# Kernel optimization log

Hardware: AMD Instinct MI355X
Metric: run time of the kernel (lower is better)

Reference implementation:

```python
import jax, jax.numpy as jnp
import numpy as np
import itertools

DIM = 384
KEY_DIM = 32
NUM_HEADS = 8
ATTN_RATIO = 4
RESOLUTION = 7
D = ATTN_RATIO * KEY_DIM          # 128
DH = D * NUM_HEADS                # 1024
H_QKV = DH + 2 * KEY_DIM * NUM_HEADS  # 1536
B = 2048
N = RESOLUTION ** 2               # 49


def _build_bias_idxs():
    points = list(itertools.product(range(RESOLUTION), range(RESOLUTION)))
    attention_offsets = {}
    idxs = []
    for p1 in points:
        for p2 in points:
            offset = (abs(p1[0] - p2[0]), abs(p1[1] - p2[1]))
            if offset not in attention_offsets:
                attention_offsets[offset] = len(attention_offsets)
            idxs.append(attention_offsets[offset])
    return np.array(idxs, dtype=np.int32).reshape(N, N), len(attention_offsets)


def setup_inputs() -> dict:
    key = jax.random.key(0)
    ks = jax.random.split(key, 6)
    bias_idxs_np, n_offsets = _build_bias_idxs()  # n_offsets == 49 for resolution 7
    x = jax.random.normal(ks[0], (B, N, DIM), dtype=jnp.float32)
    qkv_w = jax.random.normal(ks[1], (H_QKV, DIM), dtype=jnp.float32) * (DIM ** -0.5)
    qkv_b = jnp.zeros((H_QKV,), dtype=jnp.float32)
    proj_w = jax.random.normal(ks[2], (DIM, DH), dtype=jnp.float32) * (DH ** -0.5)
    proj_b = jnp.zeros((DIM,), dtype=jnp.float32)
    attn_bias = jax.random.normal(ks[3], (NUM_HEADS, n_offsets), dtype=jnp.float32) * 0.02
    bias_idxs = jnp.asarray(bias_idxs_np)
    return {"x": x, "qkv_w": qkv_w, "qkv_b": qkv_b, "proj_w": proj_w,
            "proj_b": proj_b, "attn_bias": attn_bias, "bias_idxs": bias_idxs}


def reference(x, qkv_w, qkv_b, proj_w, proj_b, attn_bias, bias_idxs):
    Bb, Nn, _ = x.shape
    scale = KEY_DIM ** -0.5
    qkv = x @ qkv_w.T + qkv_b                       # [B, N, 1536]
    qkv = qkv.reshape(Bb, Nn, NUM_HEADS, KEY_DIM + KEY_DIM + D)
    q = qkv[..., :KEY_DIM]                          # [B, N, H, kd]
    k = qkv[..., KEY_DIM:2 * KEY_DIM]               # [B, N, H, kd]
    v = qkv[..., 2 * KEY_DIM:]                      # [B, N, H, d]
    bias = attn_bias[:, bias_idxs]                  # [H, N, N] gathered rel-pos bias
    attn = jnp.einsum('bnhk,bmhk->bhnm', q, k) * scale + bias
    attn = jax.nn.softmax(attn, axis=-1)
    out = jnp.einsum('bhnm,bmhd->bnhd', attn, v).reshape(Bb, Nn, DH)
    return out @ proj_w.T + proj_b                  # [B, N, dim]
```

## Files before the change

kernel.cpp:

```cpp
#include <hip/hip_runtime.h>
#include <cstddef>
#include <cstdint>

#define TOK    49
#define KD     32
#define NH     8
#define DHEAD  128
#define HQKV   1536
#define DHTOT  1024
#define DIMM   384

typedef unsigned short u16;
typedef float  f32x4  __attribute__((ext_vector_type(4)));
typedef __bf16 bf16x8 __attribute__((ext_vector_type(8)));

typedef const __attribute__((address_space(1))) void gas_void;
typedef __attribute__((address_space(3))) void las_void;

static __device__ __forceinline__ u16 f2bf(float f) {
    unsigned int u = __builtin_bit_cast(unsigned int, f);
    return (u16)((u + 0x7fffu + ((u >> 16) & 1u)) >> 16);
}

static __device__ __forceinline__ int swz(int row, int c) {
    return (row << 6) + ((((c >> 3) ^ (row & 7)) << 3) | (c & 7));
}

static __device__ __forceinline__ int swzV(int row, int c) {
    return (row << 6) + ((((c >> 3) ^ (row & 7) ^ ((row >> 3) & 7)) << 3) | (c & 7));
}

static __device__ __forceinline__ int xcd_chunk(int bid, int nwg) {
    const int xcd = bid & 7, slot = bid >> 3;
    const int q = nwg >> 3, r = nwg & 7;
    return (xcd < r ? xcd * (q + 1) : r * (q + 1) + (xcd - r) * q) + slot;
}

#define BAR() __builtin_amdgcn_s_barrier()
#define WAIT_VM8() asm volatile("s_waitcnt vmcnt(8)" ::: "memory")
#define WAIT_VM0() asm volatile("s_waitcnt vmcnt(0)" ::: "memory")

__global__ __launch_bounds__(256)
void cast_swz(const float* __restrict__ in, u16* __restrict__ out, int K8, long nchunk)
{
    long i = (long)blockIdx.x * 256 + threadIdx.x;
    const long stride = (long)gridDim.x * 256;
    for (; i < nchunk; i += stride) {
        const long row = i / K8;
        const int  c8  = (int)(i - row * K8);
        const int  slot = c8 & 7, tpan = c8 >> 3;
        float4 v0 = reinterpret_cast<const float4*>(in)[i * 2];
        float4 v1 = reinterpret_cast<const float4*>(in)[i * 2 + 1];
        uint4 o;
        o.x = f2bf(v0.x) | ((unsigned)f2bf(v0.y) << 16);
        o.y = f2bf(v0.z) | ((unsigned)f2bf(v0.w) << 16);
        o.z = f2bf(v1.x) | ((unsigned)f2bf(v1.y) << 16);
        o.w = f2bf(v1.z) | ((unsigned)f2bf(v1.w) << 16);
        *reinterpret_cast<uint4*>(out + row * (long)K8 * 8 + tpan * 64 +
                                  ((slot ^ ((int)row & 7)) << 3)) = o;
    }
}

__global__ __launch_bounds__(256)
void bias_expand(const float* __restrict__ attn_bias, const int* __restrict__ idxs,
                 float* __restrict__ bias_full, int n_off)
{
    int i = blockIdx.x * 256 + threadIdx.x;
    if (i < NH * TOK * TOK) {
        int h = i / (TOK * TOK), s = i - h * (TOK * TOK);
        bias_full[i] = attn_bias[h * n_off + idxs[s]];
    }
}

static __device__ __forceinline__ int frag_off(int row, int ks8fg) {
    return (row << 6) + (((ks8fg ^ (row & 7)) << 3));
}

__global__ __launch_bounds__(256)
void gemm_qkv(const u16* __restrict__ A,
              const u16* __restrict__ W,
              const float* __restrict__ bias,
              u16* __restrict__ qkvb, int M)
{
    const int K = DIMM;
    const int NB = HQKV / 128;
    const int nwg = (M / 128) * NB;
    const int wgid = xcd_chunk(blockIdx.x, nwg);
    const int bm = (wgid / NB) * 128;
    const int bn = (wgid % NB) * 128;

    __shared__ u16 Alds[2][128 * 64];
    __shared__ u16 Blds[2][128 * 64];

    const int t    = threadIdx.x;
    const int lane = t & 63;
    const int wv   = t >> 6;
    const int wr   = wv >> 1;
    const int wc   = wv & 1;

    const int lrow = lane >> 3;
    const int lcol = (lane & 7) * 8;
    const int frow = lane & 15;
    const int fg   = lane >> 4;

    f32x4 acc[4][4];
    #pragma unroll
    for (int mi = 0; mi < 4; ++mi)
        #pragma unroll
        for (int ni = 0; ni < 4; ++ni) acc[mi][ni] = (f32x4)0.0f;

    auto STAGE = [&](int buf, int k0) {
        #pragma unroll
        for (int i = 0; i < 4; ++i) {
            const int c   = i * 4 + wv;
            const int row = c * 8 + lrow;
            __builtin_amdgcn_global_load_lds((gas_void*)(A + (size_t)(bm + row) * K + k0 + lcol),
                                             (las_void*)(&Alds[buf][c * 512]), 16, 0, 0);
            __builtin_amdgcn_global_load_lds((gas_void*)(W + (size_t)(bn + row) * K + k0 + lcol),
                                             (las_void*)(&Blds[buf][c * 512]), 16, 0, 0);
        }
    };

    STAGE(0, 0);
    STAGE(1, 64);

    const int NT = 6;
    for (int ts = 0; ts < NT; ++ts) {
        if (ts < NT - 1) { WAIT_VM8(); }
        else             { WAIT_VM0(); }
        BAR();
        const u16* Ab = Alds[ts & 1];
        const u16* Bb = Blds[ts & 1];
        #pragma unroll
        for (int ks = 0; ks < 2; ++ks) {
            const int sl = ks * 4 + fg;
            bf16x8 af[4], bf[4];
            #pragma unroll
            for (int mi = 0; mi < 4; ++mi)
                af[mi] = *reinterpret_cast<const bf16x8*>(&Ab[frag_off(wr * 64 + mi * 16 + frow, sl)]);
            #pragma unroll
            for (int ni = 0; ni < 4; ++ni)
                bf[ni] = *reinterpret_cast<const bf16x8*>(&Bb[frag_off(wc * 64 + ni * 16 + frow, sl)]);
            #pragma unroll
            for (int mi = 0; mi < 4; ++mi)
                #pragma unroll
                for (int ni = 0; ni < 4; ++ni)
                    acc[mi][ni] = __builtin_amdgcn_mfma_f32_16x16x32_bf16(af[mi], bf[ni], acc[mi][ni], 0, 0, 0);
        }
        BAR();
        if (ts < NT - 2) STAGE(ts & 1, (ts + 2) * 64);
    }

    const int rbase = (lane >> 4) * 4;
    #pragma unroll
    for (int ni = 0; ni < 4; ++ni) {
        const int col = bn + wc * 64 + ni * 16 + frow;
        const float bv = bias[col];
        #pragma unroll
        for (int mi = 0; mi < 4; ++mi) {
            #pragma unroll
            for (int j = 0; j < 4; ++j) {
                const int row = bm + wr * 64 + mi * 16 + rbase + j;
                qkvb[(size_t)row * HQKV + col] = f2bf(acc[mi][ni][j] + bv);
            }
        }
    }
}

__global__ __launch_bounds__(256)
void gemm_bf16_nt(const u16* __restrict__ A, const u16* __restrict__ W,
                  const float* __restrict__ bias, float* __restrict__ C,
                  int M, int N, int K)
{
    const int NB = N / 128;
    const int nwg = (M / 128) * NB;
    const int wgid = xcd_chunk(blockIdx.x, nwg);
    const int bm = (wgid / NB) * 128;
    const int bn = (wgid % NB) * 128;

    __shared__ u16 Alds[2][128 * 64];
    __shared__ u16 Blds[2][128 * 64];

    const int t    = threadIdx.x;
    const int lane = t & 63;
    const int wv   = t >> 6;
    const int wr   = wv >> 1;
    const int wc   = wv & 1;

    const int lrow = lane >> 3;
    const int lcol = (lane & 7) * 8;
    const int frow = lane & 15;
    const int fg   = lane >> 4;

    f32x4 acc[4][4];
    #pragma unroll
    for (int mi = 0; mi < 4; ++mi)
        #pragma unroll
        for (int ni = 0; ni < 4; ++ni) acc[mi][ni] = (f32x4)0.0f;

    auto STAGE = [&](int buf, int k0) {
        #pragma unroll
        for (int i = 0; i < 4; ++i) {
            const int c   = i * 4 + wv;
            const int row = c * 8 + lrow;
            __builtin_amdgcn_global_load_lds((gas_void*)(A + (size_t)(bm + row) * K + k0 + lcol),
                                             (las_void*)(&Alds[buf][c * 512]), 16, 0, 0);
            __builtin_amdgcn_global_load_lds((gas_void*)(W + (size_t)(bn + row) * K + k0 + lcol),
                                             (las_void*)(&Blds[buf][c * 512]), 16, 0, 0);
        }
    };

    const int NT = K / 64;
    STAGE(0, 0);
    STAGE(1, 64);

    for (int ts = 0; ts < NT; ++ts) {
        if (ts < NT - 1) { WAIT_VM8(); }
        else             { WAIT_VM0(); }
        BAR();
        const u16* Ab = Alds[ts & 1];
        const u16* Bb = Blds[ts & 1];
        #pragma unroll
        for (int ks = 0; ks < 2; ++ks) {
            const int sl = ks * 4 + fg;
            bf16x8 af[4], bf[4];
            #pragma unroll
            for (int mi = 0; mi < 4; ++mi)
                af[mi] = *reinterpret_cast<const bf16x8*>(&Ab[frag_off(wr * 64 + mi * 16 + frow, sl)]);
            #pragma unroll
            for (int ni = 0; ni < 4; ++ni)
                bf[ni] = *reinterpret_cast<const bf16x8*>(&Bb[frag_off(wc * 64 + ni * 16 + frow, sl)]);
            #pragma unroll
            for (int mi = 0; mi < 4; ++mi)
                #pragma unroll
                for (int ni = 0; ni < 4; ++ni)
                    acc[mi][ni] = __builtin_amdgcn_mfma_f32_16x16x32_bf16(af[mi], bf[ni], acc[mi][ni], 0, 0, 0);
        }
        BAR();
        if (ts < NT - 2) STAGE(ts & 1, (ts + 2) * 64);
    }

    const int rbase = (lane >> 4) * 4;
    #pragma unroll
    for (int ni = 0; ni < 4; ++ni) {
        const int col = bn + wc * 64 + ni * 16 + frow;
        const float bv = bias[col];
        #pragma unroll
        for (int mi = 0; mi < 4; ++mi) {
            #pragma unroll
            for (int j = 0; j < 4; ++j) {
                const int row = bm + wr * 64 + mi * 16 + rbase + j;
                C[(size_t)row * N + col] = acc[mi][ni][j] + bv;
            }
        }
    }
}

__global__ __launch_bounds__(256)
void attn_mfma(const u16* __restrict__ qkvb,
               const float* __restrict__ bias_full,
               u16* __restrict__ ab)
{
    __shared__ __align__(16) u16  QKs[64 * 64];
    __shared__ __align__(16) u16  Vts[128 * 64];
    __shared__ __align__(16) float S[64 * 80];
    __shared__ __align__(16) u16  Ps[64 * 64];

    const int t    = threadIdx.x;
    const int lane = t & 63;
    const int w    = t >> 6;
    const int fr   = lane & 15;
    const int fg   = lane >> 4;
    const int b    = blockIdx.x;
    const int h    = blockIdx.y;

    if (t < 128 * 2) {
        const int row = t >> 1, sl = 6 + (t & 1);
        *reinterpret_cast<uint4*>(&Vts[(row << 6) +
            (((sl ^ (row & 7) ^ ((row >> 3) & 7)) & 7) << 3)]) = make_uint4(0, 0, 0, 0);
    }
    __syncthreads();

    const u16* qrow = qkvb + (size_t)b * TOK * HQKV + h * 192;
    for (int flat = t; flat < TOK * 24; flat += 256) {
        const int n = flat / 24, c24 = flat - n * 24;
        uint4 u = *reinterpret_cast<const uint4*>(qrow + (size_t)n * HQKV + c24 * 8);
        if (c24 < 8) {
            *reinterpret_cast<uint4*>(&QKs[(n << 6) + ((c24 ^ (n & 7)) << 3)]) = u;
        } else {
            const int d0 = (c24 - 8) * 8;
            u16 vals[8];
            *reinterpret_cast<uint4*>(vals) = u;
            #pragma unroll
            for (int e = 0; e < 8; ++e)
                Vts[swzV(d0 + e, n)] = vals[e];
        }
    }
    __syncthreads();

    bf16x8 qf = *reinterpret_cast<const bf16x8*>(&QKs[swz(16 * w + fr, fg * 8)]);
    f32x4 sacc[4];
    #pragma unroll
    for (int nj = 0; nj < 4; ++nj) {
        bf16x8 kf = *reinterpret_cast<const bf16x8*>(&QKs[swz(16 * nj + fr, 32 + fg * 8)]);
        sacc[nj] = __builtin_amdgcn_mfma_f32_16x16x32_bf16(qf, kf, (f32x4)0.0f, 0, 0, 0);
    }

    const float scale = 0.17677669529663687f;
    const float* bh_bias = bias_full + h * (TOK * TOK);
    #pragma unroll
    for (int nj = 0; nj < 4; ++nj) {
        #pragma unroll
        for (int j = 0; j < 4; ++j) {
            const int row = 16 * w + fg * 4 + j;
            const int col = 16 * nj + fr;
            const int rn = row < TOK ? row : TOK - 1;
            const int cm = col < TOK ? col : TOK - 1;
            S[row * 80 + col] = sacc[nj][j] * scale + bh_bias[rn * TOK + cm];
        }
    }
    __syncthreads();

    {
        const int n = t >> 2, j = t & 3;
        const float* Sr = &S[n * 80];
        float v[16];
        #pragma unroll
        for (int e = 0; e < 8; ++e) v[e]     = Sr[8 * j + e];
        #pragma unroll
        for (int e = 0; e < 8; ++e) v[8 + e] = Sr[32 + 8 * j + e];

        float mx = -1e30f;
        #pragma unroll
        for (int e = 0; e < 8; ++e) mx = fmaxf(mx, v[e]);
        #pragma unroll
        for (int e = 0; e < 8; ++e)
            if (32 + 8 * j + e < TOK) mx = fmaxf(mx, v[8 + e]);
        mx = fmaxf(mx, __shfl_xor(mx, 1, 4));
        mx = fmaxf(mx, __shfl_xor(mx, 2, 4));

        float sum = 0.f;
        #pragma unroll
        for (int e = 0; e < 8; ++e) { v[e] = __expf(v[e] - mx); sum += v[e]; }
        #pragma unroll
        for (int e = 0; e < 8; ++e) {
            const float ev = (32 + 8 * j + e < TOK) ? __expf(v[8 + e] - mx) : 0.f;
            v[8 + e] = ev; sum += ev;
        }
        sum += __shfl_xor(sum, 1, 4);
        sum += __shfl_xor(sum, 2, 4);
        const float inv = 1.f / sum;

        uint4 o;
        o.x = f2bf(v[0] * inv)  | ((unsigned)f2bf(v[1] * inv)  << 16);
        o.y = f2bf(v[2] * inv)  | ((unsigned)f2bf(v[3] * inv)  << 16);
        o.z = f2bf(v[4] * inv)  | ((unsigned)f2bf(v[5] * inv)  << 16);
        o.w = f2bf(v[6] * inv)  | ((unsigned)f2bf(v[7] * inv)  << 16);
        *reinterpret_cast<uint4*>(&Ps[swz(n, 8 * j)]) = o;
        o.x = f2bf(v[8] * inv)  | ((unsigned)f2bf(v[9] * inv)  << 16);
        o.y = f2bf(v[10] * inv) | ((unsigned)f2bf(v[11] * inv) << 16);
        o.z = f2bf(v[12] * inv) | ((unsigned)f2bf(v[13] * inv) << 16);
        o.w = f2bf(v[14] * inv) | ((unsigned)f2bf(v[15] * inv) << 16);
        *reinterpret_cast<uint4*>(&Ps[swz(n, 32 + 8 * j)]) = o;
    }
    __syncthreads();

    f32x4 oacc[8];
    #pragma unroll
    for (int nj = 0; nj < 8; ++nj) oacc[nj] = (f32x4)0.0f;
    #pragma unroll
    for (int ks = 0; ks < 2; ++ks) {
        bf16x8 pf = *reinterpret_cast<const bf16x8*>(&Ps[swz(16 * w + fr, ks * 32 + fg * 8)]);
        #pragma unroll
        for (int nj = 0; nj < 8; ++nj) {
            bf16x8 vf = *reinterpret_cast<const bf16x8*>(&Vts[swzV(16 * nj + fr, ks * 32 + fg * 8)]);
            oacc[nj] = __builtin_amdgcn_mfma_f32_16x16x32_bf16(pf, vf, oacc[nj], 0, 0, 0);
        }
    }

    #pragma unroll
    for (int nj = 0; nj < 8; ++nj) {
        const int d = 16 * nj + fr;
        const int c = h * DHEAD + d;
        const int tp = c >> 6, sl = (c >> 3) & 7, cc = c & 7;
        #pragma unroll
        for (int j = 0; j < 4; ++j) {
            const int n = 16 * w + fg * 4 + j;
            if (n < TOK) {
                const int gr = b * TOK + n;
                ab[(size_t)gr * DHTOT + (tp << 6) + (((sl ^ (gr & 7)) << 3) | cc)] = f2bf(oacc[nj][j]);
            }
        }
    }
}

extern "C" void kernel_launch(void* const* d_in, const int* in_sizes, int n_in,
                              void* d_out, int out_size, void* d_ws, size_t ws_size,
                              hipStream_t stream)
{
    const float* x         = (const float*)d_in[0];
    const float* qkv_w     = (const float*)d_in[1];
    const float* qkv_b     = (const float*)d_in[2];
    const float* proj_w    = (const float*)d_in[3];
    const float* proj_b    = (const float*)d_in[4];
    const float* attn_bias = (const float*)d_in[5];
    const int*   bias_idxs = (const int*)d_in[6];

    const int Mtot  = in_sizes[0] / DIMM;
    const int Btot  = Mtot / TOK;
    const int n_off = in_sizes[5] / NH;

    const size_t nWq = (size_t)HQKV * DIMM;
    const size_t nWp = (size_t)DIMM * DHTOT;
    float* bias_full = (float*)d_ws;
    u16*   wq        = (u16*)((char*)d_ws + 76832);
    u16*   wp        = wq + nWq;
    u16*   dyn       = wp + nWp;
    const size_t fixed_bytes = 76832 + (nWq + nWp) * sizeof(u16);
    const size_t per_batch = (size_t)TOK * (DIMM + HQKV + DHTOT) * 2;

    if (ws_size <= fixed_bytes) return;
    long BcL = (long)((ws_size - fixed_bytes) / per_batch);
    int Bc = (int)((BcL / 128) * 128);
    if (Bc <= 0) return;
    if (Bc > Btot) Bc = Btot;

    cast_swz<<<dim3(288), 256, 0, stream>>>(qkv_w, wq, DIMM / 8, (long)HQKV * (DIMM / 8));
    cast_swz<<<dim3(192), 256, 0, stream>>>(proj_w, wp, DHTOT / 8, (long)DIMM * (DHTOT / 8));
    bias_expand<<<dim3((NH * TOK * TOK + 255) / 256), 256, 0, stream>>>(attn_bias, bias_idxs, bias_full, n_off);

    for (int b0 = 0; b0 < Btot; b0 += Bc) {
        const int bc = (b0 + Bc <= Btot) ? Bc : (Btot - b0);
        const int Mc = bc * TOK;

        u16* xb   = dyn;
        u16* qkvb = xb   + (size_t)Bc * TOK * DIMM;
        u16* abb  = qkvb + (size_t)Bc * TOK * HQKV;

        const float* xc   = x + (size_t)b0 * TOK * DIMM;
        float*       outc = (float*)d_out + (size_t)b0 * TOK * DIMM;

        cast_swz<<<dim3(2048), 256, 0, stream>>>(xc, xb, DIMM / 8, (long)Mc * (DIMM / 8));

        gemm_qkv<<<dim3((Mc / 128) * (HQKV / 128)), 256, 0, stream>>>(xb, wq, qkv_b, qkvb, Mc);

        attn_mfma<<<dim3(bc, NH), 256, 0, stream>>>(qkvb, bias_full, abb);

        gemm_bf16_nt<<<dim3((Mc / 128) * (DIMM / 128)), 256, 0, stream>>>(abb, wp, proj_b, outc, Mc, DIMM, DHTOT);
    }
}
```

Measured before the change: 682.8 us.

## Process all heads per attention block with double-buffered register prefetch

The attention kernel now launches one block per batch element instead of one per (batch, head) and loops over the eight heads. Each head's Q/K/V loads are prefetched into registers while the previous head is computed, and the shared-memory tiles are double-buffered. Barriers become explicit lgkmcnt waits plus s_barrier. This aims to hide global-load latency and cut per-block setup cost. In exchange it uses more LDS per block and launches eight times fewer blocks, which lowers occupancy and available parallelism.

```diff
diff --git a/kernel.cpp b/kernel.cpp
--- a/kernel.cpp
+++ b/kernel.cpp
@@ -39,6 +39,8 @@
 #define BAR() __builtin_amdgcn_s_barrier()
 #define WAIT_VM8() asm volatile("s_waitcnt vmcnt(8)" ::: "memory")
 #define WAIT_VM0() asm volatile("s_waitcnt vmcnt(0)" ::: "memory")
+#define LGKM0_BAR() do { asm volatile("s_waitcnt lgkmcnt(0)" ::: "memory"); \
+                         __builtin_amdgcn_s_barrier(); } while (0)
 
 __global__ __launch_bounds__(256)
 void cast_swz(const float* __restrict__ in, u16* __restrict__ out, int K8, long nchunk)
@@ -256,58 +258,64 @@
     }
 }
 
-__global__ __launch_bounds__(256)
-void attn_mfma(const u16* __restrict__ qkvb,
-               const float* __restrict__ bias_full,
-               u16* __restrict__ ab)
-{
-    __shared__ __align__(16) u16  QKs[64 * 64];
-    __shared__ __align__(16) u16  Vts[128 * 64];
-    __shared__ __align__(16) float S[64 * 80];
-    __shared__ __align__(16) u16  Ps[64 * 64];
-
-    const int t    = threadIdx.x;
+#define NCH 5
+
+struct Regs { uint4 v[NCH]; };
+
+static __device__ __forceinline__ void load_regs(Regs& r, const u16* __restrict__ base, int t)
+{
+    #pragma unroll
+    for (int k = 0; k < NCH; ++k) {
+        const int idx = t + k * 256;
+        if (idx < TOK * 24) {
+            const int n = idx / 24, c = idx - n * 24;
+            r.v[k] = *reinterpret_cast<const uint4*>(base + (size_t)n * HQKV + c * 8);
+        }
+    }
+}
+
+static __device__ __forceinline__ void write_lds(const Regs& r, u16* __restrict__ QK,
+                                                 u16* __restrict__ V, int t)
+{
+    #pragma unroll
+    for (int k = 0; k < NCH; ++k) {
+        const int idx = t + k * 256;
+        if (idx < TOK * 24) {
+            const int n = idx / 24, c24 = idx - n * 24;
+            if (c24 < 8) {
+                *reinterpret_cast<uint4*>(&QK[(n << 6) + ((c24 ^ (n & 7)) << 3)]) = r.v[k];
+            } else {
+                const int d0 = (c24 - 8) * 8;
+                u16 vals[8];
+                *reinterpret_cast<uint4*>(vals) = r.v[k];
+                #pragma unroll
+                for (int e = 0; e < 8; ++e)
+                    V[swzV(d0 + e, n)] = vals[e];
+            }
+        }
+    }
+}
+
+static __device__ __forceinline__ void attn_head(
+    const u16* __restrict__ QK, const u16* __restrict__ V,
+    float* __restrict__ S, u16* __restrict__ Ps,
+    const float* __restrict__ bh_bias, u16* __restrict__ ab,
+    int b, int h, int t)
+{
     const int lane = t & 63;
     const int w    = t >> 6;
     const int fr   = lane & 15;
     const int fg   = lane >> 4;
-    const int b    = blockIdx.x;
-    const int h    = blockIdx.y;
-
-    if (t < 128 * 2) {
-        const int row = t >> 1, sl = 6 + (t & 1);
-        *reinterpret_cast<uint4*>(&Vts[(row << 6) +
-            (((sl ^ (row & 7) ^ ((row >> 3) & 7)) & 7) << 3)]) = make_uint4(0, 0, 0, 0);
-    }
-    __syncthreads();
-
-    const u16* qrow = qkvb + (size_t)b * TOK * HQKV + h * 192;
-    for (int flat = t; flat < TOK * 24; flat += 256) {
-        const int n = flat / 24, c24 = flat - n * 24;
-        uint4 u = *reinterpret_cast<const uint4*>(qrow + (size_t)n * HQKV + c24 * 8);
-        if (c24 < 8) {
-            *reinterpret_cast<uint4*>(&QKs[(n << 6) + ((c24 ^ (n & 7)) << 3)]) = u;
-        } else {
-            const int d0 = (c24 - 8) * 8;
-            u16 vals[8];
-            *reinterpret_cast<uint4*>(vals) = u;
-            #pragma unroll
-            for (int e = 0; e < 8; ++e)
-                Vts[swzV(d0 + e, n)] = vals[e];
-        }
-    }
-    __syncthreads();
-
-    bf16x8 qf = *reinterpret_cast<const bf16x8*>(&QKs[swz(16 * w + fr, fg * 8)]);
+
+    bf16x8 qf = *reinterpret_cast<const bf16x8*>(&QK[swz(16 * w + fr, fg * 8)]);
     f32x4 sacc[4];
     #pragma unroll
     for (int nj = 0; nj < 4; ++nj) {
-        bf16x8 kf = *reinterpret_cast<const bf16x8*>(&QKs[swz(16 * nj + fr, 32 + fg * 8)]);
+        bf16x8 kf = *reinterpret_cast<const bf16x8*>(&QK[swz(16 * nj + fr, 32 + fg * 8)]);
         sacc[nj] = __builtin_amdgcn_mfma_f32_16x16x32_bf16(qf, kf, (f32x4)0.0f, 0, 0, 0);
     }
 
     const float scale = 0.17677669529663687f;
-    const float* bh_bias = bias_full + h * (TOK * TOK);
     #pragma unroll
     for (int nj = 0; nj < 4; ++nj) {
         #pragma unroll
@@ -319,7 +327,7 @@
             S[row * 80 + col] = sacc[nj][j] * scale + bh_bias[rn * TOK + cm];
         }
     }
-    __syncthreads();
+    LGKM0_BAR();
 
     {
         const int n = t >> 2, j = t & 3;
@@ -363,7 +371,7 @@
         o.w = f2bf(v[14] * inv) | ((unsigned)f2bf(v[15] * inv) << 16);
         *reinterpret_cast<uint4*>(&Ps[swz(n, 32 + 8 * j)]) = o;
     }
-    __syncthreads();
+    LGKM0_BAR();
 
     f32x4 oacc[8];
     #pragma unroll
@@ -373,7 +381,7 @@
         bf16x8 pf = *reinterpret_cast<const bf16x8*>(&Ps[swz(16 * w + fr, ks * 32 + fg * 8)]);
         #pragma unroll
         for (int nj = 0; nj < 8; ++nj) {
-            bf16x8 vf = *reinterpret_cast<const bf16x8*>(&Vts[swzV(16 * nj + fr, ks * 32 + fg * 8)]);
+            bf16x8 vf = *reinterpret_cast<const bf16x8*>(&V[swzV(16 * nj + fr, ks * 32 + fg * 8)]);
             oacc[nj] = __builtin_amdgcn_mfma_f32_16x16x32_bf16(pf, vf, oacc[nj], 0, 0, 0);
         }
     }
@@ -391,6 +399,46 @@
                 ab[(size_t)gr * DHTOT + (tp << 6) + (((sl ^ (gr & 7)) << 3) | cc)] = f2bf(oacc[nj][j]);
             }
         }
+    }
+}
+
+__global__ __launch_bounds__(256)
+void attn_mfma(const u16* __restrict__ qkvb,
+               const float* __restrict__ bias_full,
+               u16* __restrict__ ab)
+{
+    __shared__ __align__(16) u16  QKs[2][64 * 64];
+    __shared__ __align__(16) u16  Vts[2][128 * 64];
+    __shared__ __align__(16) float S[64 * 80];
+    __shared__ __align__(16) u16  Ps[64 * 64];
+
+    const int t = threadIdx.x;
+    const int b = blockIdx.x;
+    const u16* base = qkvb + (size_t)b * TOK * HQKV;
+
+    Regs ra, rb;
+    load_regs(ra, base + 0 * 192, t);
+
+    for (int i = t; i < 128 * 2 * 2; i += 256) {
+        const int bufi = i >> 9, r = (i >> 1) & 127, sl = 6 + (i & 1);
+        *reinterpret_cast<uint4*>(&Vts[bufi][(r << 6) +
+            (((sl ^ (r & 7) ^ ((r >> 3) & 7)) & 7) << 3)]) = make_uint4(0, 0, 0, 0);
+    }
+    LGKM0_BAR();
+
+    #pragma unroll
+    for (int hp = 0; hp < 4; ++hp) {
+        const int h0 = hp * 2, h1 = hp * 2 + 1;
+
+        write_lds(ra, QKs[0], Vts[0], t);
+        load_regs(rb, base + h1 * 192, t);
+        LGKM0_BAR();
+        attn_head(QKs[0], Vts[0], S, Ps, bias_full + h0 * (TOK * TOK), ab, b, h0, t);
+
+        write_lds(rb, QKs[1], Vts[1], t);
+        if (hp < 3) load_regs(ra, base + (h0 + 2) * 192, t);
+        LGKM0_BAR();
+        attn_head(QKs[1], Vts[1], S, Ps, bias_full + h1 * (TOK * TOK), ab, b, h1, t);
     }
 }
 
@@ -444,7 +492,7 @@
 
         gemm_qkv<<<dim3((Mc / 128) * (HQKV / 128)), 256, 0, stream>>>(xb, wq, qkv_b, qkvb, Mc);
 
-        attn_mfma<<<dim3(bc, NH), 256, 0, stream>>>(qkvb, bias_full, abb);
+        attn_mfma<<<dim3(bc), 256, 0, stream>>>(qkvb, bias_full, abb);
 
         gemm_bf16_nt<<<dim3((Mc / 128) * (DIMM / 128)), 256, 0, stream>>>(abb, wp, proj_b, outc, Mc, DIMM, DHTOT);
     }
```

Result: slower. 725.3 us (+6.2%).

## Fuse output projection into attention kernel, looping heads per block

Applied to the files above, without the earlier changes.

Attention and the output projection GEMM now run in one kernel. Each block handles one batch element, loops over all 8 heads, stages the per-head output in LDS reused from the score buffer, and accumulates the projection directly from proj weights read from global memory. This removes the bf16 attention-output round trip through global memory and one kernel launch per chunk, and frees workspace so chunks can be larger. In exchange, the grid shrinks from batch×heads to batch blocks with a serial head loop and uncached global weight fragment loads, which may lower parallelism and occupancy.

```diff
diff --git a/kernel.cpp b/kernel.cpp
--- a/kernel.cpp
+++ b/kernel.cpp
@@ -30,6 +30,10 @@
     return (row << 6) + ((((c >> 3) ^ (row & 7) ^ ((row >> 3) & 7)) << 3) | (c & 7));
 }
 
+static __device__ __forceinline__ int swzO(int row, int c) {
+    return (row << 7) + ((((c >> 3) ^ (row & 7) ^ ((row >> 2) & 7)) << 3) | (c & 7));
+}
+
 static __device__ __forceinline__ int xcd_chunk(int bid, int nwg) {
     const int xcd = bid & 7, slot = bid >> 3;
     const int q = nwg >> 3, r = nwg & 7;
@@ -39,6 +43,8 @@
 #define BAR() __builtin_amdgcn_s_barrier()
 #define WAIT_VM8() asm volatile("s_waitcnt vmcnt(8)" ::: "memory")
 #define WAIT_VM0() asm volatile("s_waitcnt vmcnt(0)" ::: "memory")
+#define LGKM0_BAR() do { asm volatile("s_waitcnt lgkmcnt(0)" ::: "memory"); \
+                         __builtin_amdgcn_s_barrier(); } while (0)
 
 __global__ __launch_bounds__(256)
 void cast_swz(const float* __restrict__ in, u16* __restrict__ out, int K8, long nchunk)
@@ -62,6 +68,23 @@
 }
 
 __global__ __launch_bounds__(256)
+void cast_plain(const float* __restrict__ in, u16* __restrict__ out, long n8)
+{
+    long i = (long)blockIdx.x * 256 + threadIdx.x;
+    const long stride = (long)gridDim.x * 256;
+    for (; i < n8; i += stride) {
+        float4 v0 = reinterpret_cast<const float4*>(in)[i * 2];
+        float4 v1 = reinterpret_cast<const float4*>(in)[i * 2 + 1];
+        uint4 o;
+        o.x = f2bf(v0.x) | ((unsigned)f2bf(v0.y) << 16);
+        o.y = f2bf(v0.z) | ((unsigned)f2bf(v0.w) << 16);
+        o.z = f2bf(v1.x) | ((unsigned)f2bf(v1.y) << 16);
+        o.w = f2bf(v1.z) | ((unsigned)f2bf(v1.w) << 16);
+        reinterpret_cast<uint4*>(out)[i] = o;
+    }
+}
+
+__global__ __launch_bounds__(256)
 void bias_expand(const float* __restrict__ attn_bias, const int* __restrict__ idxs,
                  float* __restrict__ bias_full, int n_off)
 {
@@ -168,103 +191,19 @@
 }
 
 __global__ __launch_bounds__(256)
-void gemm_bf16_nt(const u16* __restrict__ A, const u16* __restrict__ W,
-                  const float* __restrict__ bias, float* __restrict__ C,
-                  int M, int N, int K)
-{
-    const int NB = N / 128;
-    const int nwg = (M / 128) * NB;
-    const int wgid = xcd_chunk(blockIdx.x, nwg);
-    const int bm = (wgid / NB) * 128;
-    const int bn = (wgid % NB) * 128;
-
-    __shared__ u16 Alds[2][128 * 64];
-    __shared__ u16 Blds[2][128 * 64];
-
-    const int t    = threadIdx.x;
-    const int lane = t & 63;
-    const int wv   = t >> 6;
-    const int wr   = wv >> 1;
-    const int wc   = wv & 1;
-
-    const int lrow = lane >> 3;
-    const int lcol = (lane & 7) * 8;
-    const int frow = lane & 15;
-    const int fg   = lane >> 4;
-
-    f32x4 acc[4][4];
-    #pragma unroll
-    for (int mi = 0; mi < 4; ++mi)
-        #pragma unroll
-        for (int ni = 0; ni < 4; ++ni) acc[mi][ni] = (f32x4)0.0f;
-
-    auto STAGE = [&](int buf, int k0) {
-        #pragma unroll
-        for (int i = 0; i < 4; ++i) {
-            const int c   = i * 4 + wv;
-            const int row = c * 8 + lrow;
-            __builtin_amdgcn_global_load_lds((gas_void*)(A + (size_t)(bm + row) * K + k0 + lcol),
-                                             (las_void*)(&Alds[buf][c * 512]), 16, 0, 0);
-            __builtin_amdgcn_global_load_lds((gas_void*)(W + (size_t)(bn + row) * K + k0 + lcol),
-                                             (las_void*)(&Blds[buf][c * 512]), 16, 0, 0);
-        }
-    };
-
-    const int NT = K / 64;
-    STAGE(0, 0);
-    STAGE(1, 64);
-
-    for (int ts = 0; ts < NT; ++ts) {
-        if (ts < NT - 1) { WAIT_VM8(); }
-        else             { WAIT_VM0(); }
-        BAR();
-        const u16* Ab = Alds[ts & 1];
-        const u16* Bb = Blds[ts & 1];
-        #pragma unroll
-        for (int ks = 0; ks < 2; ++ks) {
-            const int sl = ks * 4 + fg;
-            bf16x8 af[4], bf[4];
-            #pragma unroll
-            for (int mi = 0; mi < 4; ++mi)
-                af[mi] = *reinterpret_cast<const bf16x8*>(&Ab[frag_off(wr * 64 + mi * 16 + frow, sl)]);
-            #pragma unroll
-            for (int ni = 0; ni < 4; ++ni)
-                bf[ni] = *reinterpret_cast<const bf16x8*>(&Bb[frag_off(wc * 64 + ni * 16 + frow, sl)]);
-            #pragma unroll
-            for (int mi = 0; mi < 4; ++mi)
-                #pragma unroll
-                for (int ni = 0; ni < 4; ++ni)
-                    acc[mi][ni] = __builtin_amdgcn_mfma_f32_16x16x32_bf16(af[mi], bf[ni], acc[mi][ni], 0, 0, 0);
-        }
-        BAR();
-        if (ts < NT - 2) STAGE(ts & 1, (ts + 2) * 64);
-    }
-
-    const int rbase = (lane >> 4) * 4;
-    #pragma unroll
-    for (int ni = 0; ni < 4; ++ni) {
-        const int col = bn + wc * 64 + ni * 16 + frow;
-        const float bv = bias[col];
-        #pragma unroll
-        for (int mi = 0; mi < 4; ++mi) {
-            #pragma unroll
-            for (int j = 0; j < 4; ++j) {
-                const int row = bm + wr * 64 + mi * 16 + rbase + j;
-                C[(size_t)row * N + col] = acc[mi][ni][j] + bv;
-            }
-        }
-    }
-}
-
-__global__ __launch_bounds__(256)
-void attn_mfma(const u16* __restrict__ qkvb,
+void attn_proj(const u16* __restrict__ qkvb,
+               const u16* __restrict__ wp,
+               const float* __restrict__ proj_b,
                const float* __restrict__ bias_full,
-               u16* __restrict__ ab)
+               float* __restrict__ out)
 {
     __shared__ __align__(16) u16  QKs[64 * 64];
     __shared__ __align__(16) u16  Vts[128 * 64];
-    __shared__ __align__(16) float S[64 * 80];
+    __shared__ __align__(16) unsigned char SU[64 * 80 * 4];
     __shared__ __align__(16) u16  Ps[64 * 64];
+
+    float* S  = reinterpret_cast<float*>(SU);
+    u16*   Os = reinterpret_cast<u16*>(SU);
 
     const int t    = threadIdx.x;
     const int lane = t & 63;
@@ -272,123 +211,163 @@
     const int fr   = lane & 15;
     const int fg   = lane >> 4;
     const int b    = blockIdx.x;
-    const int h    = blockIdx.y;
+
+    const u16* base = qkvb + (size_t)b * TOK * HQKV;
+    const float scale = 0.17677669529663687f;
+
+    f32x4 pacc[4][6];
+    #pragma unroll
+    for (int mf = 0; mf < 4; ++mf)
+        #pragma unroll
+        for (int nc = 0; nc < 6; ++nc) pacc[mf][nc] = (f32x4)0.0f;
 
     if (t < 128 * 2) {
         const int row = t >> 1, sl = 6 + (t & 1);
         *reinterpret_cast<uint4*>(&Vts[(row << 6) +
             (((sl ^ (row & 7) ^ ((row >> 3) & 7)) & 7) << 3)]) = make_uint4(0, 0, 0, 0);
     }
-    __syncthreads();
-
-    const u16* qrow = qkvb + (size_t)b * TOK * HQKV + h * 192;
-    for (int flat = t; flat < TOK * 24; flat += 256) {
-        const int n = flat / 24, c24 = flat - n * 24;
-        uint4 u = *reinterpret_cast<const uint4*>(qrow + (size_t)n * HQKV + c24 * 8);
-        if (c24 < 8) {
-            *reinterpret_cast<uint4*>(&QKs[(n << 6) + ((c24 ^ (n & 7)) << 3)]) = u;
-        } else {
-            const int d0 = (c24 - 8) * 8;
-            u16 vals[8];
-            *reinterpret_cast<uint4*>(vals) = u;
+    LGKM0_BAR();
+
+    #pragma unroll 1
+    for (int h = 0; h < NH; ++h) {
+        const u16* qrow = base + h * 192;
+        for (int flat = t; flat < TOK * 24; flat += 256) {
+            const int n = flat / 24, c24 = flat - n * 24;
+            uint4 u = *reinterpret_cast<const uint4*>(qrow + (size_t)n * HQKV + c24 * 8);
+            if (c24 < 8) {
+                *reinterpret_cast<uint4*>(&QKs[(n << 6) + ((c24 ^ (n & 7)) << 3)]) = u;
+            } else {
+                const int d0 = (c24 - 8) * 8;
+                u16 vals[8];
+                *reinterpret_cast<uint4*>(vals) = u;
+                #pragma unroll
+                for (int e = 0; e < 8; ++e)
+                    Vts[swzV(d0 + e, n)] = vals[e];
+            }
+        }
+        LGKM0_BAR();
+
+        bf16x8 qf = *reinterpret_cast<const bf16x8*>(&QKs[swz(16 * w + fr, fg * 8)]);
+        f32x4 sacc[4];
+        #pragma unroll
+        for (int nj = 0; nj < 4; ++nj) {
+            bf16x8 kf = *reinterpret_cast<const bf16x8*>(&QKs[swz(16 * nj + fr, 32 + fg * 8)]);
+            sacc[nj] = __builtin_amdgcn_mfma_f32_16x16x32_bf16(qf, kf, (f32x4)0.0f, 0, 0, 0);
+        }
+        const float* bh_bias = bias_full + h * (TOK * TOK);
+        #pragma unroll
+        for (int nj = 0; nj < 4; ++nj) {
+            #pragma unroll
+            for (int j = 0; j < 4; ++j) {
+                const int row = 16 * w + fg * 4 + j;
+                const int col = 16 * nj + fr;
+                const int rn = row < TOK ? row : TOK - 1;
+                const int cm = col < TOK ? col : TOK - 1;
+                S[row * 80 + col] = sacc[nj][j] * scale + bh_bias[rn * TOK + cm];
+            }
+        }
+        LGKM0_BAR();
+
+        {
+            const int n = t >> 2, j = t & 3;
+            const float* Sr = &S[n * 80];
+            float v[16];
+            #pragma unroll
+            for (int e = 0; e < 8; ++e) v[e]     = Sr[8 * j + e];
+            #pragma unroll
+            for (int e = 0; e < 8; ++e) v[8 + e] = Sr[32 + 8 * j + e];
+
+            float mx = -1e30f;
+            #pragma unroll
+            for (int e = 0; e < 8; ++e) mx = fmaxf(mx, v[e]);
             #pragma unroll
             for (int e = 0; e < 8; ++e)
-                Vts[swzV(d0 + e, n)] = vals[e];
-        }
-    }
-    __syncthreads();
-
-    bf16x8 qf = *reinterpret_cast<const bf16x8*>(&QKs[swz(16 * w + fr, fg * 8)]);
-    f32x4 sacc[4];
+                if (32 + 8 * j + e < TOK) mx = fmaxf(mx, v[8 + e]);
+            mx = fmaxf(mx, __shfl_xor(mx, 1, 4));
+            mx = fmaxf(mx, __shfl_xor(mx, 2, 4));
+
+            float sum = 0.f;
+            #pragma unroll
+            for (int e = 0; e < 8; ++e) { v[e] = __expf(v[e] - mx); sum += v[e]; }
+            #pragma unroll
+            for (int e = 0; e < 8; ++e) {
+                const float ev = (32 + 8 * j + e < TOK) ? __expf(v[8 + e] - mx) : 0.f;
+                v[8 + e] = ev; sum += ev;
+            }
+            sum += __shfl_xor(sum, 1, 4);
+            sum += __shfl_xor(sum, 2, 4);
+            const float inv = 1.f / sum;
+
+            uint4 o;
+            o.x = f2bf(v[0] * inv)  | ((unsigned)f2bf(v[1] * inv)  << 16);
+            o.y = f2bf(v[2] * inv)  | ((unsigned)f2bf(v[3] * inv)  << 16);
+            o.z = f2bf(v[4] * inv)  | ((unsigned)f2bf(v[5] * inv)  << 16);
+            o.w = f2bf(v[6] * inv)  | ((unsigned)f2bf(v[7] * inv)  << 16);
+            *reinterpret_cast<uint4*>(&Ps[swz(n, 8 * j)]) = o;
+            o.x = f2bf(v[8] * inv)  | ((unsigned)f2bf(v[9] * inv)  << 16);
+            o.y = f2bf(v[10] * inv) | ((unsigned)f2bf(v[11] * inv) << 16);
+            o.z = f2bf(v[12] * inv) | ((unsigned)f2bf(v[13] * inv) << 16);
+            o.w = f2bf(v[14] * inv) | ((unsigned)f2bf(v[15] * inv) << 16);
+            *reinterpret_cast<uint4*>(&Ps[swz(n, 32 + 8 * j)]) = o;
+        }
+        LGKM0_BAR();
+
+        f32x4 oacc[8];
+        #pragma unroll
+        for (int nj = 0; nj < 8; ++nj) oacc[nj] = (f32x4)0.0f;
+        #pragma unroll
+        for (int ks = 0; ks < 2; ++ks) {
+            bf16x8 pf = *reinterpret_cast<const bf16x8*>(&Ps[swz(16 * w + fr, ks * 32 + fg * 8)]);
+            #pragma unroll
+            for (int nj = 0; nj < 8; ++nj) {
+                bf16x8 vf = *reinterpret_cast<const bf16x8*>(&Vts[swzV(16 * nj + fr, ks * 32 + fg * 8)]);
+                oacc[nj] = __builtin_amdgcn_mfma_f32_16x16x32_bf16(pf, vf, oacc[nj], 0, 0, 0);
+            }
+        }
+
+        #pragma unroll
+        for (int nj = 0; nj < 8; ++nj) {
+            #pragma unroll
+            for (int j = 0; j < 4; ++j) {
+                const int n = 16 * w + fg * 4 + j;
+                Os[swzO(n, 16 * nj + fr)] = f2bf(oacc[nj][j]);
+            }
+        }
+        LGKM0_BAR();
+
+        const u16* wph = wp + h * DHEAD;
+        #pragma unroll
+        for (int ks = 0; ks < 4; ++ks) {
+            bf16x8 bfr[6];
+            #pragma unroll
+            for (int nc = 0; nc < 6; ++nc) {
+                const int col = w * 96 + nc * 16 + fr;
+                bfr[nc] = *reinterpret_cast<const bf16x8*>(wph + (size_t)col * DHTOT + ks * 32 + fg * 8);
+            }
+            bf16x8 afr[4];
+            #pragma unroll
+            for (int mf = 0; mf < 4; ++mf)
+                afr[mf] = *reinterpret_cast<const bf16x8*>(&Os[swzO(16 * mf + fr, ks * 32 + fg * 8)]);
+            #pragma unroll
+            for (int mf = 0; mf < 4; ++mf)
+                #pragma unroll
+                for (int nc = 0; nc < 6; ++nc)
+                    pacc[mf][nc] = __builtin_amdgcn_mfma_f32_16x16x32_bf16(afr[mf], bfr[nc], pacc[mf][nc], 0, 0, 0);
+        }
+        LGKM0_BAR();
+    }
+
     #pragma unroll
-    for (int nj = 0; nj < 4; ++nj) {
-        bf16x8 kf = *reinterpret_cast<const bf16x8*>(&QKs[swz(16 * nj + fr, 32 + fg * 8)]);
-        sacc[nj] = __builtin_amdgcn_mfma_f32_16x16x32_bf16(qf, kf, (f32x4)0.0f, 0, 0, 0);
-    }
-
-    const float scale = 0.17677669529663687f;
-    const float* bh_bias = bias_full + h * (TOK * TOK);
-    #pragma unroll
-    for (int nj = 0; nj < 4; ++nj) {
-        #pragma unroll
-        for (int j = 0; j < 4; ++j) {
-            const int row = 16 * w + fg * 4 + j;
-            const int col = 16 * nj + fr;
-            const int rn = row < TOK ? row : TOK - 1;
-            const int cm = col < TOK ? col : TOK - 1;
-            S[row * 80 + col] = sacc[nj][j] * scale + bh_bias[rn * TOK + cm];
-        }
-    }
-    __syncthreads();
-
-    {
-        const int n = t >> 2, j = t & 3;
-        const float* Sr = &S[n * 80];
-        float v[16];
-        #pragma unroll
-        for (int e = 0; e < 8; ++e) v[e]     = Sr[8 * j + e];
-        #pragma unroll
-        for (int e = 0; e < 8; ++e) v[8 + e] = Sr[32 + 8 * j + e];
-
-        float mx = -1e30f;
-        #pragma unroll
-        for (int e = 0; e < 8; ++e) mx = fmaxf(mx, v[e]);
-        #pragma unroll
-        for (int e = 0; e < 8; ++e)
-            if (32 + 8 * j + e < TOK) mx = fmaxf(mx, v[8 + e]);
-        mx = fmaxf(mx, __shfl_xor(mx, 1, 4));
-        mx = fmaxf(mx, __shfl_xor(mx, 2, 4));
-
-        float sum = 0.f;
-        #pragma unroll
-        for (int e = 0; e < 8; ++e) { v[e] = __expf(v[e] - mx); sum += v[e]; }
-        #pragma unroll
-        for (int e = 0; e < 8; ++e) {
-            const float ev = (32 + 8 * j + e < TOK) ? __expf(v[8 + e] - mx) : 0.f;
-            v[8 + e] = ev; sum += ev;
-        }
-        sum += __shfl_xor(sum, 1, 4);
-        sum += __shfl_xor(sum, 2, 4);
-        const float inv = 1.f / sum;
-
-        uint4 o;
-        o.x = f2bf(v[0] * inv)  | ((unsigned)f2bf(v[1] * inv)  << 16);
-        o.y = f2bf(v[2] * inv)  | ((unsigned)f2bf(v[3] * inv)  << 16);
-        o.z = f2bf(v[4] * inv)  | ((unsigned)f2bf(v[5] * inv)  << 16);
-        o.w = f2bf(v[6] * inv)  | ((unsigned)f2bf(v[7] * inv)  << 16);
-        *reinterpret_cast<uint4*>(&Ps[swz(n, 8 * j)]) = o;
-        o.x = f2bf(v[8] * inv)  | ((unsigned)f2bf(v[9] * inv)  << 16);
-        o.y = f2bf(v[10] * inv) | ((unsigned)f2bf(v[11] * inv) << 16);
-        o.z = f2bf(v[12] * inv) | ((unsigned)f2bf(v[13] * inv) << 16);
-        o.w = f2bf(v[14] * inv) | ((unsigned)f2bf(v[15] * inv) << 16);
-        *reinterpret_cast<uint4*>(&Ps[swz(n, 32 + 8 * j)]) = o;
-    }
-    __syncthreads();
-
-    f32x4 oacc[8];
-    #pragma unroll
-    for (int nj = 0; nj < 8; ++nj) oacc[nj] = (f32x4)0.0f;
-    #pragma unroll
-    for (int ks = 0; ks < 2; ++ks) {
-        bf16x8 pf = *reinterpret_cast<const bf16x8*>(&Ps[swz(16 * w + fr, ks * 32 + fg * 8)]);
-        #pragma unroll
-        for (int nj = 0; nj < 8; ++nj) {
-            bf16x8 vf = *reinterpret_cast<const bf16x8*>(&Vts[swzV(16 * nj + fr, ks * 32 + fg * 8)]);
-            oacc[nj] = __builtin_amdgcn_mfma_f32_16x16x32_bf16(pf, vf, oacc[nj], 0, 0, 0);
-        }
-    }
-
-    #pragma unroll
-    for (int nj = 0; nj < 8; ++nj) {
-        const int d = 16 * nj + fr;
-        const int c = h * DHEAD + d;
-        const int tp = c >> 6, sl = (c >> 3) & 7, cc = c & 7;
-        #pragma unroll
-        for (int j = 0; j < 4; ++j) {
-            const int n = 16 * w + fg * 4 + j;
-            if (n < TOK) {
-                const int gr = b * TOK + n;
-                ab[(size_t)gr * DHTOT + (tp << 6) + (((sl ^ (gr & 7)) << 3) | cc)] = f2bf(oacc[nj][j]);
+    for (int nc = 0; nc < 6; ++nc) {
+        const int col = w * 96 + nc * 16 + fr;
+        const float bv = proj_b[col];
+        #pragma unroll
+        for (int mf = 0; mf < 4; ++mf) {
+            #pragma unroll
+            for (int j = 0; j < 4; ++j) {
+                const int row = 16 * mf + fg * 4 + j;
+                if (row < TOK)
+                    out[((size_t)b * TOK + row) * DIMM + col] = pacc[mf][nc][j] + bv;
             }
         }
     }
@@ -417,7 +396,7 @@
     u16*   wp        = wq + nWq;
     u16*   dyn       = wp + nWp;
     const size_t fixed_bytes = 76832 + (nWq + nWp) * sizeof(u16);
-    const size_t per_batch = (size_t)TOK * (DIMM + HQKV + DHTOT) * 2;
+    const size_t per_batch = (size_t)TOK * (DIMM + HQKV) * 2;
 
     if (ws_size <= fixed_bytes) return;
     long BcL = (long)((ws_size - fixed_bytes) / per_batch);
@@ -426,7 +405,7 @@
     if (Bc > Btot) Bc = Btot;
 
     cast_swz<<<dim3(288), 256, 0, stream>>>(qkv_w, wq, DIMM / 8, (long)HQKV * (DIMM / 8));
-    cast_swz<<<dim3(192), 256, 0, stream>>>(proj_w, wp, DHTOT / 8, (long)DIMM * (DHTOT / 8));
+    cast_plain<<<dim3(192), 256, 0, stream>>>(proj_w, wp, (long)(DIMM * DHTOT / 8));
     bias_expand<<<dim3((NH * TOK * TOK + 255) / 256), 256, 0, stream>>>(attn_bias, bias_idxs, bias_full, n_off);
 
     for (int b0 = 0; b0 < Btot; b0 += Bc) {
@@ -434,8 +413,7 @@
         const int Mc = bc * TOK;
 
         u16* xb   = dyn;
-        u16* qkvb = xb   + (size_t)Bc * TOK * DIMM;
-        u16* abb  = qkvb + (size_t)Bc * TOK * HQKV;
+        u16* qkvb = xb + (size_t)Bc * TOK * DIMM;
 
         const float* xc   = x + (size_t)b0 * TOK * DIMM;
         float*       outc = (float*)d_out + (size_t)b0 * TOK * DIMM;
@@ -444,8 +422,6 @@
 
         gemm_qkv<<<dim3((Mc / 128) * (HQKV / 128)), 256, 0, stream>>>(xb, wq, qkv_b, qkvb, Mc);
 
-        attn_mfma<<<dim3(bc, NH), 256, 0, stream>>>(qkvb, bias_full, abb);
-
-        gemm_bf16_nt<<<dim3((Mc / 128) * (DIMM / 128)), 256, 0, stream>>>(abb, wp, proj_b, outc, Mc, DIMM, DHTOT);
-    }
-}
+        attn_proj<<<dim3(bc), 256, 0, stream>>>(qkvb, wp, proj_b, bias_full, outc);
+    }
+}
```

New measurement: 854.1 us. 1.25x slower.
